# Kernel tuning notes

Measured on AMD Instinct MI355X. Metric: run time of the kernel, lower is better.

## Reference

```python
import jax, jax.numpy as jnp
import numpy as np

HEADS = 8
DIM_HEAD = 64
DIM = 512
CTX_DIM = 512
INNER = HEADS * DIM_HEAD  # 512
EPS = 1e-5


def layernorm(x, g):
    # repo-style LayerNorm: learnable gain g only, no bias, biased variance
    mean = jnp.mean(x, axis=-1, keepdims=True)
    var = jnp.var(x, axis=-1, keepdims=True)
    return (x - mean) * jax.lax.rsqrt(var + EPS) * g


def setup_inputs() -> dict:
    key = jax.random.key(0)
    ks = jax.random.split(key, 8)
    b, n, m = 2, 4096, 4096
    x = jax.random.normal(ks[0], (b, n, DIM), dtype=jnp.float32)
    context = jax.random.normal(ks[1], (b, m, CTX_DIM), dtype=jnp.float32)
    mask = jax.random.bernoulli(ks[2], 0.9, (b, m))  # bool [b, m]
    # parameters
    g_x = jnp.ones((DIM,), dtype=jnp.float32)
    null_kv = jax.random.normal(ks[3], (2, DIM_HEAD), dtype=jnp.float32)
    Wq = jax.random.normal(ks[4], (DIM, INNER), dtype=jnp.float32) * (DIM ** -0.5)
    Wkv = jax.random.normal(ks[5], (CTX_DIM, 2 * INNER), dtype=jnp.float32) * (CTX_DIM ** -0.5)
    Wo = jax.random.normal(ks[6], (INNER, DIM), dtype=jnp.float32) * (INNER ** -0.5)
    g_out = jnp.ones((DIM,), dtype=jnp.float32)
    return {"x": x, "context": context, "mask": mask, "g_x": g_x,
            "null_kv": null_kv, "Wq": Wq, "Wkv": Wkv, "Wo": Wo, "g_out": g_out}


def reference(x, context, mask, g_x, null_kv, Wq, Wkv, Wo, g_out):
    b, n, _ = x.shape
    m = context.shape[1]
    scale = DIM_HEAD ** (-0.5)  # cosine_sim=False

    xn = layernorm(x, g_x)
    ctx = context  # norm_context=False -> Identity

    q = (xn @ Wq).reshape(b, n, HEADS, DIM_HEAD)          # b n h d
    kv = (ctx @ Wkv).reshape(b, m, 2, HEADS, DIM_HEAD)     # b m 2 h d
    k, v = kv[:, :, 0], kv[:, :, 1]                        # b m h d

    # prepend the null kv token (shared across b, h)
    nk = jnp.broadcast_to(null_kv[0], (b, 1, HEADS, DIM_HEAD))
    nv = jnp.broadcast_to(null_kv[1], (b, 1, HEADS, DIM_HEAD))
    k = jnp.concatenate([nk, k], axis=1)                   # b (m+1) h d
    v = jnp.concatenate([nv, v], axis=1)

    s = jnp.sqrt(jnp.float32(scale))
    q = q * s
    k = k * s

    sim = jnp.einsum('bihd,bjhd->bhij', q, k)              # b h n (m+1)
    max_neg = -jnp.finfo(sim.dtype).max
    full_mask = jnp.pad(mask, ((0, 0), (1, 0)), constant_values=True)  # null token visible
    sim = jnp.where(full_mask[:, None, None, :], sim, max_neg)

    attn = jax.nn.softmax(sim.astype(jnp.float32), axis=-1).astype(sim.dtype)
    out = jnp.einsum('bhij,bjhd->bihd', attn, v).reshape(b, n, INNER)
    out = out @ Wo
    return layernorm(out, g_out)
```

## Files before the change

### kernel.cpp

```cpp
#include <hip/hip_runtime.h>
#include <cfloat>

typedef unsigned short u16;
typedef unsigned int u32;
typedef __bf16 v8bf16 __attribute__((ext_vector_type(8)));
typedef float v4f32 __attribute__((ext_vector_type(4)));
typedef float v16f32 __attribute__((ext_vector_type(16)));

#define MPAD 4224
#define QKS 0.42466090f
#define GRPS 1024

__device__ __forceinline__ u16 f2bf(float f) {
  union { float f; u32 u; } v; v.f = f;
  u32 u = v.u;
  u32 r = (u + 0x7FFFu + ((u >> 16) & 1u)) >> 16;
  return (u16)r;
}

__device__ __forceinline__ u32 pkbf(float lo, float hi) {
  union { float f; u32 u; } a, c;
  a.f = lo; c.f = hi;
  return __builtin_amdgcn_perm(c.u, a.u, 0x07060302);
}

__device__ __forceinline__ float asf(u32 u) {
  union { u32 u; float f; } v; v.u = u; return v.f;
}

__device__ __forceinline__ void exppack2(v16f32& sA, v16f32& sB, float& lst,
                                         v8bf16 pf[4]) {
  float rsum = 0.f;
#pragma unroll
  for (int i = 0; i < 16; i++) { float p = __builtin_amdgcn_exp2f(sA[i]); sA[i] = p; rsum += p; }
#pragma unroll
  for (int i = 0; i < 16; i++) { float p = __builtin_amdgcn_exp2f(sB[i]); sB[i] = p; rsum += p; }
  float a2 = rsum, b2 = rsum;
  asm("v_permlane32_swap_b32 %0, %1" : "+v"(a2), "+v"(b2));
  lst += a2 + b2;
#pragma unroll
  for (int kc = 0; kc < 2; kc++) {
    v16f32& s = kc ? sB : sA;
#pragma unroll
    for (int s16 = 0; s16 < 2; s16++) {
      u32 w0 = pkbf(s[s16 * 8 + 0], s[s16 * 8 + 1]);
      u32 w1 = pkbf(s[s16 * 8 + 2], s[s16 * 8 + 3]);
      u32 w2 = pkbf(s[s16 * 8 + 4], s[s16 * 8 + 5]);
      u32 w3 = pkbf(s[s16 * 8 + 6], s[s16 * 8 + 7]);
      asm("v_permlane32_swap_b32 %0, %1" : "+v"(w0), "+v"(w2));
      asm("v_permlane32_swap_b32 %0, %1" : "+v"(w1), "+v"(w3));
      union { u32 u[4]; v8bf16 v; } pu;
      pu.u[0] = w0; pu.u[1] = w1; pu.u[2] = w2; pu.u[3] = w3;
      pf[kc * 2 + s16] = pu.v;
    }
  }
}

__global__ __launch_bounds__(256) void transpose_cast3(const float* __restrict__ Wq,
    const float* __restrict__ Wkv, const float* __restrict__ Wo,
    u16* __restrict__ WqT, u16* __restrict__ WkvT, u16* __restrict__ WoT) {
  __shared__ float tile[32][33];
  int bb = blockIdx.x;
  const float* in; u16* out; int N; float scale; int base;
  if (bb < 256)      { in = Wq;  out = WqT;  N = 512;  scale = QKS; base = bb; }
  else if (bb < 768) { in = Wkv; out = WkvT; N = 1024; scale = 1.f; base = bb - 256; }
  else               { in = Wo;  out = WoT;  N = 512;  scale = 1.f; base = bb - 768; }
  const int K = 512;
  int ntiles = N >> 5;
  int bx = base % ntiles, by = base / ntiles;
  int n0 = bx * 32, k0 = by * 32;
  int c = threadIdx.x & 31, r8 = threadIdx.x >> 5;
#pragma unroll
  for (int i = 0; i < 4; i++) {
    int r = r8 + i * 8;
    tile[r][c] = in[(size_t)(k0 + r) * N + n0 + c];
  }
  __syncthreads();
#pragma unroll
  for (int i = 0; i < 4; i++) {
    int r = r8 + i * 8;
    out[(size_t)(n0 + r) * K + k0 + c] = f2bf(tile[c][r] * scale);
  }
}

__global__ __launch_bounds__(256) void ln_to_bf16(const float* __restrict__ in,
    const float* __restrict__ g, u16* __restrict__ out) {
  int lane = threadIdx.x & 63, w = threadIdx.x >> 6;
  int row = blockIdx.x * 4 + w;
  const float* p = in + (size_t)row * 512 + lane * 8;
  float4 f0 = *(const float4*)p;
  float4 f1 = *(const float4*)(p + 4);
  float v[8] = {f0.x, f0.y, f0.z, f0.w, f1.x, f1.y, f1.z, f1.w};
  float sum = 0.f, sq = 0.f;
#pragma unroll
  for (int i = 0; i < 8; i++) { sum += v[i]; sq += v[i] * v[i]; }
#pragma unroll
  for (int m = 1; m < 64; m <<= 1) { sum += __shfl_xor(sum, m); sq += __shfl_xor(sq, m); }
  float mean = sum * (1.f / 512.f);
  float var = sq * (1.f / 512.f) - mean * mean;
  float rstd = rsqrtf(var + 1e-5f);
  const float* gp = g + lane * 8;
  u16 o[8];
#pragma unroll
  for (int i = 0; i < 8; i++) o[i] = f2bf((v[i] - mean) * rstd * gp[i]);
  *(uint4*)&out[(size_t)row * 512 + lane * 8] = *(uint4*)o;
}

__global__ __launch_bounds__(256) void ln_to_f32(const float* __restrict__ in,
    const float* __restrict__ g, float* __restrict__ out) {
  int lane = threadIdx.x & 63, w = threadIdx.x >> 6;
  int row = blockIdx.x * 4 + w;
  const float* p = in + (size_t)row * 512 + lane * 8;
  float4 f0 = *(const float4*)p;
  float4 f1 = *(const float4*)(p + 4);
  float v[8] = {f0.x, f0.y, f0.z, f0.w, f1.x, f1.y, f1.z, f1.w};
  float sum = 0.f, sq = 0.f;
#pragma unroll
  for (int i = 0; i < 8; i++) { sum += v[i]; sq += v[i] * v[i]; }
#pragma unroll
  for (int m = 1; m < 64; m <<= 1) { sum += __shfl_xor(sum, m); sq += __shfl_xor(sq, m); }
  float mean = sum * (1.f / 512.f);
  float var = sq * (1.f / 512.f) - mean * mean;
  float rstd = rsqrtf(var + 1e-5f);
  const float* gp = g + lane * 8;
  float o[8];
#pragma unroll
  for (int i = 0; i < 8; i++) o[i] = (v[i] - mean) * rstd * gp[i];
  float* q = out + (size_t)row * 512 + lane * 8;
  *(float4*)q = make_float4(o[0], o[1], o[2], o[3]);
  *(float4*)(q + 4) = make_float4(o[4], o[5], o[6], o[7]);
}

__global__ __launch_bounds__(256) void cast_f32_bf16(const float4* __restrict__ in,
    u16* __restrict__ out, int n4) {
  int i = blockIdx.x * 256 + threadIdx.x;
  if (i >= n4) return;
  float4 f = in[i];
  u16 o[4] = {f2bf(f.x), f2bf(f.y), f2bf(f.z), f2bf(f.w)};
  *(uint2*)&out[i * 4] = *(uint2*)o;
}

__global__ void detect_mask_dtype(const unsigned char* __restrict__ m, int* __restrict__ flag) {
  int i = blockIdx.x * 256 + threadIdx.x;
  if (i < 8192 && (i & 3) && m[i]) atomicOr(flag, 1);
}

__global__ void build_maskpad(const void* __restrict__ mask, const int* __restrict__ flag,
    float* __restrict__ mp) {
  int i = blockIdx.x * 256 + threadIdx.x;
  if (i >= 2 * MPAD) return;
  int b = i / MPAD, p = i - b * MPAD;
  float v;
  if (p == 0) v = 0.f;
  else if (p <= 4096) {
    int j = b * 4096 + (p - 1);
    int on = (*flag) ? (((const unsigned char*)mask)[j] != 0)
                     : (((const int*)mask)[j] != 0);
    v = on ? 0.f : -1e38f;
  } else v = -1e38f;
  mp[i] = v;
}

__global__ __launch_bounds__(256) void fill_extras(const float* __restrict__ nullkv,
    u16* __restrict__ KVt) {
  int bh = blockIdx.x, tid = threadIdx.x;
  size_t tb64 = ((size_t)bh * 66 + 64) * 8192;
  uint4 z = make_uint4(0, 0, 0, 0);
  for (int i = tid; i < 2048; i += 256)
    *(uint4*)&KVt[tb64 + (size_t)i * 8] = z;
  size_t tb0 = (size_t)bh * 66 * 8192;
  if (tid < 64) {
    int d = tid;
    KVt[tb0 + (size_t)(d >> 3) * 512 + (d & 7)] = f2bf(nullkv[d] * QKS);
    KVt[tb0 + 4096 + (size_t)d * 8] = f2bf(nullkv[64 + d]);
  }
}

__global__ __launch_bounds__(256) void gemm_bf16(const u16* __restrict__ A,
    const u16* __restrict__ Bt, u16* __restrict__ outb, float* __restrict__ outf,
    u16* __restrict__ KVt, int Ncols, int mode) {
  __shared__ __attribute__((aligned(16))) u16 As[128 * 32];
  __shared__ __attribute__((aligned(16))) u16 Bs[128 * 32];
  int tiles_n = Ncols >> 7;
  int n0 = (blockIdx.x % tiles_n) * 128;
  int m0 = (blockIdx.x / tiles_n) * 128;
  int tid = threadIdx.x;
  int lane = tid & 63, w = tid >> 6, quad = lane >> 4, l15 = lane & 15;
  int wr = w >> 1, wc = w & 1;
  int srow = tid >> 2, scol = (tid & 3) * 8;
  v4f32 acc[4][4];
#pragma unroll
  for (int i = 0; i < 4; i++)
#pragma unroll
    for (int j = 0; j < 4; j++) acc[i][j] = (v4f32){0.f, 0.f, 0.f, 0.f};

  for (int k0 = 0; k0 < 512; k0 += 32) {
    __syncthreads();
    __builtin_amdgcn_global_load_lds((const u32*)&A[(size_t)(m0 + srow) * 512 + k0 + scol],
                                     (u32*)&As[tid * 8], 16, 0, 0);
    __builtin_amdgcn_global_load_lds((const u32*)&A[(size_t)(m0 + 64 + srow) * 512 + k0 + scol],
                                     (u32*)&As[64 * 32 + tid * 8], 16, 0, 0);
    __builtin_amdgcn_global_load_lds((const u32*)&Bt[(size_t)(n0 + srow) * 512 + k0 + scol],
                                     (u32*)&Bs[tid * 8], 16, 0, 0);
    __builtin_amdgcn_global_load_lds((const u32*)&Bt[(size_t)(n0 + 64 + srow) * 512 + k0 + scol],
                                     (u32*)&Bs[64 * 32 + tid * 8], 16, 0, 0);
    __syncthreads();
    v8bf16 af[4], bf[4];
#pragma unroll
    for (int i = 0; i < 4; i++)
      af[i] = *(const v8bf16*)&As[(wr * 64 + i * 16 + l15) * 32 + quad * 8];
#pragma unroll
    for (int j = 0; j < 4; j++)
      bf[j] = *(const v8bf16*)&Bs[(wc * 64 + j * 16 + l15) * 32 + quad * 8];
#pragma unroll
    for (int i = 0; i < 4; i++)
#pragma unroll
      for (int j = 0; j < 4; j++)
        acc[i][j] = __builtin_amdgcn_mfma_f32_16x16x32_bf16(af[i], bf[j], acc[i][j], 0, 0, 0);
  }
#pragma unroll
  for (int i = 0; i < 4; i++) {
    int rbase = m0 + wr * 64 + i * 16 + quad * 4;
#pragma unroll
    for (int j = 0; j < 4; j++) {
      int col = n0 + wc * 64 + j * 16 + l15;
#pragma unroll
      for (int r = 0; r < 4; r++) {
        float v = acc[i][j][r];
        int row = rbase + r;
        if (mode == 0) {
          outb[(size_t)row * 512 + col] = f2bf(v);
        } else if (mode == 2) {
          outf[(size_t)row * 512 + col] = v;
        } else {
          int b2 = row >> 12, mr = row & 4095;
          int kk = mr + 1, kt = kk >> 6, kl = kk & 63;
          int kvsel = col >> 9, hh = (col >> 6) & 7, d = col & 63;
          size_t tb = ((size_t)(b2 * 8 + hh) * 66 + kt) * 8192;
          if (kvsel == 0) {
            int chunk = (((d >> 4) * 2 + ((d >> 3) & 1)) * 2 + (kl >> 5)) * 32 + (kl & 31);
            KVt[tb + (size_t)chunk * 8 + (d & 7)] = f2bf(v * QKS);
          } else {
            int chunk = (((kl >> 4) * 2 + ((kl >> 3) & 1)) * 2 + (d >> 5)) * 32 + (d & 31);
            KVt[tb + 4096 + (size_t)chunk * 8 + (kl & 7)] = f2bf(v);
          }
        }
      }
    }
  }
}

__global__ __launch_bounds__(256, 2) void attn_kernel(const u16* __restrict__ q,
    const u16* __restrict__ KVt, const float* __restrict__ maskbias,
    u32* __restrict__ Opart, float* __restrict__ lbuf) {
  int bid = blockIdx.x;
  int qt = bid & 15, bhs = bid >> 4;
  int s_p = bhs & 1, bh = bhs >> 1;
  int b = bh >> 3, hh = bh & 7;
  int tid = threadIdx.x, lane = tid & 63, w = tid >> 6;
  int m31 = lane & 31, h = (lane >> 5) & 1;
  int grp = (bh * 16 + qt) * 4 + w;
  int q0 = qt * 256 + w * 64;

  v8bf16 qf[2][4];
#pragma unroll
  for (int qg = 0; qg < 2; qg++) {
    const u16* qp = q + (size_t)(b * 4096 + q0 + qg * 32 + m31) * 512 + hh * 64 + h * 8;
#pragma unroll
    for (int ks = 0; ks < 4; ks++) qf[qg][ks] = *(const v8bf16*)&qp[ks * 16];
  }

  v16f32 acc[2][2];
#pragma unroll
  for (int qg = 0; qg < 2; qg++)
#pragma unroll
    for (int db = 0; db < 2; db++)
#pragma unroll
      for (int i = 0; i < 16; i++) acc[qg][db][i] = 0.f;
  float l_st[2] = {0.f, 0.f};

  const u16* kvb = KVt + (size_t)bh * 66 * 8192 + (size_t)(h * 64 + m31) * 8;
  const float* mg = maskbias + b * MPAD;
  int kt0 = s_p * 33;

  v8bf16 kf[4][2];
  v16f32 bs0, bs1;
  {
    const u16* tb0 = kvb + (size_t)kt0 * 8192;
#pragma unroll
    for (int ks = 0; ks < 4; ks++)
#pragma unroll
      for (int kc = 0; kc < 2; kc++)
        kf[ks][kc] = *(const v8bf16*)&tb0[ks * 1024 + kc * 256];
#pragma unroll
    for (int gg = 0; gg < 4; gg++) {
      float4 b0 = *(const float4*)&mg[kt0 * 64 + gg * 8 + h * 4];
      float4 b1 = *(const float4*)&mg[kt0 * 64 + 32 + gg * 8 + h * 4];
      bs0[gg * 4 + 0] = b0.x; bs0[gg * 4 + 1] = b0.y; bs0[gg * 4 + 2] = b0.z; bs0[gg * 4 + 3] = b0.w;
      bs1[gg * 4 + 0] = b1.x; bs1[gg * 4 + 1] = b1.y; bs1[gg * 4 + 2] = b1.z; bs1[gg * 4 + 3] = b1.w;
    }
  }

  for (int kt = kt0; kt < kt0 + 33; ++kt) {
    const u16* tb = kvb + (size_t)kt * 8192;
    int ktn = (kt + 1 < kt0 + 33) ? kt + 1 : kt0;
    const u16* tbn = kvb + (size_t)ktn * 8192;

    v8bf16 pf[2][4];

    v16f32 s0 = bs0, s1 = bs1;
#pragma unroll
    for (int ks = 0; ks < 4; ks++) {
      s0 = __builtin_amdgcn_mfma_f32_32x32x16_bf16(kf[ks][0], qf[0][ks], s0, 0, 0, 0);
      s1 = __builtin_amdgcn_mfma_f32_32x32x16_bf16(kf[ks][1], qf[0][ks], s1, 0, 0, 0);
    }

    v8bf16 vf[4][2];
#pragma unroll
    for (int jb = 0; jb < 4; jb++)
#pragma unroll
      for (int db = 0; db < 2; db++)
        vf[jb][db] = *(const v8bf16*)&tb[4096 + jb * 1024 + db * 256];

    exppack2(s0, s1, l_st[0], pf[0]);

#pragma unroll
    for (int ks = 0; ks < 4; ks++) {
      bs0 = __builtin_amdgcn_mfma_f32_32x32x16_bf16(kf[ks][0], qf[1][ks], bs0, 0, 0, 0);
      bs1 = __builtin_amdgcn_mfma_f32_32x32x16_bf16(kf[ks][1], qf[1][ks], bs1, 0, 0, 0);
    }

    v8bf16 kfn[4][2];
#pragma unroll
    for (int ks = 0; ks < 4; ks++)
#pragma unroll
      for (int kc = 0; kc < 2; kc++)
        kfn[ks][kc] = *(const v8bf16*)&tbn[ks * 1024 + kc * 256];
    v16f32 nb0, nb1;
#pragma unroll
    for (int gg = 0; gg < 4; gg++) {
      float4 b0 = *(const float4*)&mg[ktn * 64 + gg * 8 + h * 4];
      float4 b1 = *(const float4*)&mg[ktn * 64 + 32 + gg * 8 + h * 4];
      nb0[gg * 4 + 0] = b0.x; nb0[gg * 4 + 1] = b0.y; nb0[gg * 4 + 2] = b0.z; nb0[gg * 4 + 3] = b0.w;
      nb1[gg * 4 + 0] = b1.x; nb1[gg * 4 + 1] = b1.y; nb1[gg * 4 + 2] = b1.z; nb1[gg * 4 + 3] = b1.w;
    }

    exppack2(bs0, bs1, l_st[1], pf[1]);

#pragma unroll
    for (int qg = 0; qg < 2; qg++)
#pragma unroll
      for (int jb = 0; jb < 4; jb++)
#pragma unroll
        for (int db = 0; db < 2; db++)
          acc[qg][db] = __builtin_amdgcn_mfma_f32_32x32x16_bf16(vf[jb][db], pf[qg][jb], acc[qg][db], 0, 0, 0);

#pragma unroll
    for (int ks = 0; ks < 4; ks++)
#pragma unroll
      for (int kc = 0; kc < 2; kc++)
        kf[ks][kc] = kfn[ks][kc];
    bs0 = nb0; bs1 = nb1;
  }

  size_t ob = (size_t)(s_p * GRPS + grp) * 2048;
#pragma unroll
  for (int qg = 0; qg < 2; qg++)
#pragma unroll
    for (int db = 0; db < 2; db++)
#pragma unroll
      for (int rp = 0; rp < 8; rp++)
        Opart[ob + qg * 1024 + (size_t)(db * 8 + rp) * 64 + lane] =
            pkbf(acc[qg][db][2 * rp], acc[qg][db][2 * rp + 1]);
  if (h == 0) {
    lbuf[(size_t)(s_p * GRPS + grp) * 64 + m31] = l_st[0];
    lbuf[(size_t)(s_p * GRPS + grp) * 64 + 32 + m31] = l_st[1];
  }
}

__global__ __launch_bounds__(256) void attn_combine(const u32* __restrict__ Opart,
    const float* __restrict__ lbuf, u16* __restrict__ attnO) {
  __shared__ __attribute__((aligned(16))) u16 tl[4][2176];
  int tid = threadIdx.x, lane = tid & 63, w4 = tid >> 6;
  int m31 = lane & 31, h = (lane >> 5) & 1;
  int gq = blockIdx.x * 4 + w4;
  int qg = gq & 1, grp = gq >> 1;
  int w = grp & 3, qt = (grp >> 2) & 15, bh = grp >> 6;
  int b = bh >> 3, hh = bh & 7;

  float l0 = lbuf[(size_t)grp * 64 + qg * 32 + m31];
  float l1 = lbuf[(size_t)(GRPS + grp) * 64 + qg * 32 + m31];
  float inv = 1.f / (l0 + l1);

#pragma unroll
  for (int db = 0; db < 2; db++)
#pragma unroll
    for (int rp = 0; rp < 8; rp++) {
      u32 a = Opart[(size_t)grp * 2048 + qg * 1024 + (db * 8 + rp) * 64 + lane];
      u32 c = Opart[(size_t)(GRPS + grp) * 2048 + qg * 1024 + (db * 8 + rp) * 64 + lane];
      float fe = (asf(a << 16) + asf(c << 16)) * inv;
      float fo = (asf(a & 0xFFFF0000u) + asf(c & 0xFFFF0000u)) * inv;
      int reg = 2 * rp;
      int d0 = (reg & 3) + 8 * (reg >> 2) + 4 * h + 32 * db;
      *(u32*)&tl[w4][m31 * 68 + d0] = pkbf(fe, fo);
    }
  __builtin_amdgcn_s_waitcnt(0);
  int q0 = qt * 256 + w * 64 + qg * 32;
#pragma unroll
  for (int t2 = 0; t2 < 4; t2++) {
    int row = t2 * 8 + (lane >> 3), ch = lane & 7;
    uint4 val = *(uint4*)&tl[w4][row * 68 + ch * 8];
    *(uint4*)&attnO[(size_t)(b * 4096 + q0 + row) * 512 + hh * 64 + ch * 8] = val;
  }
}

extern "C" void kernel_launch(void* const* d_in, const int* in_sizes, int n_in,
                              void* d_out, int out_size, void* d_ws, size_t ws_size,
                              hipStream_t stream) {
  const float* x       = (const float*)d_in[0];
  const float* context = (const float*)d_in[1];
  const void*  mask    = d_in[2];
  const float* g_x     = (const float*)d_in[3];
  const float* null_kv = (const float*)d_in[4];
  const float* Wq      = (const float*)d_in[5];
  const float* Wkv     = (const float*)d_in[6];
  const float* Wo      = (const float*)d_in[7];
  const float* g_out   = (const float*)d_in[8];

  char* w = (char*)d_ws;
  size_t off = 0;
  auto alloc = [&](size_t bytes) { size_t o = off; off = (off + bytes + 255) & ~(size_t)255; return o; };

  u16* WqT    = (u16*)(w + alloc((size_t)512 * 512 * 2));
  u16* WkvT   = (u16*)(w + alloc((size_t)1024 * 512 * 2));
  u16* WoT    = (u16*)(w + alloc((size_t)512 * 512 * 2));
  float* mp   = (float*)(w + alloc((size_t)2 * MPAD * 4));
  int* flag   = (int*)(w + alloc(256));
  u16* KVt    = (u16*)(w + alloc((size_t)16 * 66 * 8192 * 2));
  u16* qb     = (u16*)(w + alloc((size_t)8192 * 512 * 2));
  u16* aO     = (u16*)(w + alloc((size_t)8192 * 512 * 2));
  size_t xn_off = alloc((size_t)8192 * 512 * 2);
  size_t cb_off = alloc((size_t)8192 * 512 * 2);
  float* lbb  = (float*)(w + alloc((size_t)2 * GRPS * 64 * 4));
  u16* xn   = (u16*)(w + xn_off);
  u16* cb   = (u16*)(w + cb_off);
  u32* Opart = (u32*)(w + xn_off);
  float* OP  = (float*)(w + xn_off);

  hipMemsetAsync(flag, 0, 4, stream);
  detect_mask_dtype<<<32, 256, 0, stream>>>((const unsigned char*)mask, flag);
  build_maskpad<<<(2 * MPAD + 255) / 256, 256, 0, stream>>>(mask, flag, mp);

  transpose_cast3<<<1024, 256, 0, stream>>>(Wq, Wkv, Wo, WqT, WkvT, WoT);

  ln_to_bf16<<<2048, 256, 0, stream>>>(x, g_x, xn);
  cast_f32_bf16<<<4096, 256, 0, stream>>>((const float4*)context, cb, 8192 * 512 / 4);
  fill_extras<<<16, 256, 0, stream>>>(null_kv, KVt);

  gemm_bf16<<<(8192 / 128) * (512 / 128), 256, 0, stream>>>(xn, WqT, qb, nullptr, nullptr, 512, 0);
  gemm_bf16<<<(8192 / 128) * (1024 / 128), 256, 0, stream>>>(cb, WkvT, nullptr, nullptr, KVt, 1024, 1);

  attn_kernel<<<512, 256, 0, stream>>>(qb, KVt, mp, Opart, lbb);
  attn_combine<<<512, 256, 0, stream>>>(Opart, lbb, aO);

  gemm_bf16<<<(8192 / 128) * (512 / 128), 256, 0, stream>>>(aO, WoT, nullptr, OP, nullptr, 512, 2);
  ln_to_f32<<<2048, 256, 0, stream>>>(OP, g_out, (float*)d_out);
}
```

Measured before the change: 278.9 us.

## Merge prep kernels, fuse Q/KV GEMMs, drop attention prefetch, remap attention blocks

Seven small preprocessing launches plus a memset are merged into one multi-role kernel, and each block now detects the mask dtype locally instead of using a global atomic flag. The Q and KV projection GEMMs become a single launch. The attention kernel drops its software prefetch of the next K tile and mask bias, loading them inside the loop instead, and remaps block indices so neighbouring blocks spread across batch/head. The aim is to cut launch overhead and improve scheduling, at the risk of exposing load latency in the attention loop.

```diff
diff --git a/kernel.cpp b/kernel.cpp
--- a/kernel.cpp
+++ b/kernel.cpp
@@ -56,54 +56,106 @@
   }
 }
 
-__global__ __launch_bounds__(256) void transpose_cast3(const float* __restrict__ Wq,
-    const float* __restrict__ Wkv, const float* __restrict__ Wo,
-    u16* __restrict__ WqT, u16* __restrict__ WkvT, u16* __restrict__ WoT) {
-  __shared__ float tile[32][33];
+__global__ __launch_bounds__(256) void prep_all(
+    const void* __restrict__ mask, float* __restrict__ mp,
+    const float* __restrict__ Wq, const float* __restrict__ Wkv,
+    const float* __restrict__ Wo, u16* __restrict__ WqT,
+    u16* __restrict__ WkvT, u16* __restrict__ WoT,
+    const float* __restrict__ x, const float* __restrict__ g,
+    u16* __restrict__ xn, const float4* __restrict__ ctx, u16* __restrict__ cb,
+    const float* __restrict__ nullkv, u16* __restrict__ KVt) {
   int bb = blockIdx.x;
-  const float* in; u16* out; int N; float scale; int base;
-  if (bb < 256)      { in = Wq;  out = WqT;  N = 512;  scale = QKS; base = bb; }
-  else if (bb < 768) { in = Wkv; out = WkvT; N = 1024; scale = 1.f; base = bb - 256; }
-  else               { in = Wo;  out = WoT;  N = 512;  scale = 1.f; base = bb - 768; }
-  const int K = 512;
-  int ntiles = N >> 5;
-  int bx = base % ntiles, by = base / ntiles;
-  int n0 = bx * 32, k0 = by * 32;
-  int c = threadIdx.x & 31, r8 = threadIdx.x >> 5;
-#pragma unroll
-  for (int i = 0; i < 4; i++) {
-    int r = r8 + i * 8;
-    tile[r][c] = in[(size_t)(k0 + r) * N + n0 + c];
-  }
-  __syncthreads();
-#pragma unroll
-  for (int i = 0; i < 4; i++) {
-    int r = r8 + i * 8;
-    out[(size_t)(n0 + r) * K + k0 + c] = f2bf(tile[c][r] * scale);
-  }
-}
-
-__global__ __launch_bounds__(256) void ln_to_bf16(const float* __restrict__ in,
-    const float* __restrict__ g, u16* __restrict__ out) {
-  int lane = threadIdx.x & 63, w = threadIdx.x >> 6;
-  int row = blockIdx.x * 4 + w;
-  const float* p = in + (size_t)row * 512 + lane * 8;
-  float4 f0 = *(const float4*)p;
-  float4 f1 = *(const float4*)(p + 4);
-  float v[8] = {f0.x, f0.y, f0.z, f0.w, f1.x, f1.y, f1.z, f1.w};
-  float sum = 0.f, sq = 0.f;
-#pragma unroll
-  for (int i = 0; i < 8; i++) { sum += v[i]; sq += v[i] * v[i]; }
-#pragma unroll
-  for (int m = 1; m < 64; m <<= 1) { sum += __shfl_xor(sum, m); sq += __shfl_xor(sq, m); }
-  float mean = sum * (1.f / 512.f);
-  float var = sq * (1.f / 512.f) - mean * mean;
-  float rstd = rsqrtf(var + 1e-5f);
-  const float* gp = g + lane * 8;
-  u16 o[8];
-#pragma unroll
-  for (int i = 0; i < 8; i++) o[i] = f2bf((v[i] - mean) * rstd * gp[i]);
-  *(uint4*)&out[(size_t)row * 512 + lane * 8] = *(uint4*)o;
+  int tid = threadIdx.x;
+  if (bb < 33) {
+    __shared__ int sflag;
+    if (tid == 0) sflag = 0;
+    __syncthreads();
+    const unsigned char* mb = (const unsigned char*)mask;
+    int loc = 0;
+#pragma unroll
+    for (int k = 0; k < 32; k++) {
+      int i = tid * 32 + k;
+      if ((i & 3) && mb[i]) loc = 1;
+    }
+    if (loc) sflag = 1;
+    __syncthreads();
+    int isbyte = sflag;
+    int i = bb * 256 + tid;
+    if (i >= 2 * MPAD) return;
+    int b = i / MPAD, p = i - b * MPAD;
+    float v;
+    if (p == 0) v = 0.f;
+    else if (p <= 4096) {
+      int j = b * 4096 + (p - 1);
+      int on = isbyte ? (((const unsigned char*)mask)[j] != 0)
+                      : (((const int*)mask)[j] != 0);
+      v = on ? 0.f : -1e38f;
+    } else v = -1e38f;
+    mp[i] = v;
+  } else if (bb < 1057) {
+    __shared__ float tile[32][33];
+    int t = bb - 33;
+    const float* in; u16* out; int N; float scale; int base;
+    if (t < 256)      { in = Wq;  out = WqT;  N = 512;  scale = QKS; base = t; }
+    else if (t < 768) { in = Wkv; out = WkvT; N = 1024; scale = 1.f; base = t - 256; }
+    else              { in = Wo;  out = WoT;  N = 512;  scale = 1.f; base = t - 768; }
+    const int K = 512;
+    int ntiles = N >> 5;
+    int bx = base % ntiles, by = base / ntiles;
+    int n0 = bx * 32, k0 = by * 32;
+    int c = tid & 31, r8 = tid >> 5;
+#pragma unroll
+    for (int i = 0; i < 4; i++) {
+      int r = r8 + i * 8;
+      tile[r][c] = in[(size_t)(k0 + r) * N + n0 + c];
+    }
+    __syncthreads();
+#pragma unroll
+    for (int i = 0; i < 4; i++) {
+      int r = r8 + i * 8;
+      out[(size_t)(n0 + r) * K + k0 + c] = f2bf(tile[c][r] * scale);
+    }
+  } else if (bb < 7201) {
+    int local = bb - 1057;
+    if (local < 2048) {
+      int lane = tid & 63, w = tid >> 6;
+      int row = local * 4 + w;
+      const float* p = x + (size_t)row * 512 + lane * 8;
+      float4 f0 = *(const float4*)p;
+      float4 f1 = *(const float4*)(p + 4);
+      float v[8] = {f0.x, f0.y, f0.z, f0.w, f1.x, f1.y, f1.z, f1.w};
+      float sum = 0.f, sq = 0.f;
+#pragma unroll
+      for (int i = 0; i < 8; i++) { sum += v[i]; sq += v[i] * v[i]; }
+#pragma unroll
+      for (int m = 1; m < 64; m <<= 1) { sum += __shfl_xor(sum, m); sq += __shfl_xor(sq, m); }
+      float mean = sum * (1.f / 512.f);
+      float var = sq * (1.f / 512.f) - mean * mean;
+      float rstd = rsqrtf(var + 1e-5f);
+      const float* gp = g + lane * 8;
+      u16 o[8];
+#pragma unroll
+      for (int i = 0; i < 8; i++) o[i] = f2bf((v[i] - mean) * rstd * gp[i]);
+      *(uint4*)&xn[(size_t)row * 512 + lane * 8] = *(uint4*)o;
+    } else {
+      int i = (local - 2048) * 256 + tid;
+      float4 f = ctx[i];
+      u16 o[4] = {f2bf(f.x), f2bf(f.y), f2bf(f.z), f2bf(f.w)};
+      *(uint2*)&cb[(size_t)i * 4] = *(uint2*)o;
+    }
+  } else {
+    int bh = bb - 7201;
+    size_t tb64 = ((size_t)bh * 66 + 64) * 8192;
+    uint4 z = make_uint4(0, 0, 0, 0);
+    for (int i = tid; i < 2048; i += 256)
+      *(uint4*)&KVt[tb64 + (size_t)i * 8] = z;
+    size_t tb0 = (size_t)bh * 66 * 8192;
+    if (tid < 64) {
+      int d = tid;
+      KVt[tb0 + (size_t)(d >> 3) * 512 + (d & 7)] = f2bf(nullkv[d] * QKS);
+      KVt[tb0 + 4096 + (size_t)d * 8] = f2bf(nullkv[64 + d]);
+    }
+  }
 }
 
 __global__ __launch_bounds__(256) void ln_to_f32(const float* __restrict__ in,
@@ -131,59 +183,13 @@
   *(float4*)(q + 4) = make_float4(o[4], o[5], o[6], o[7]);
 }
 
-__global__ __launch_bounds__(256) void cast_f32_bf16(const float4* __restrict__ in,
-    u16* __restrict__ out, int n4) {
-  int i = blockIdx.x * 256 + threadIdx.x;
-  if (i >= n4) return;
-  float4 f = in[i];
-  u16 o[4] = {f2bf(f.x), f2bf(f.y), f2bf(f.z), f2bf(f.w)};
-  *(uint2*)&out[i * 4] = *(uint2*)o;
-}
-
-__global__ void detect_mask_dtype(const unsigned char* __restrict__ m, int* __restrict__ flag) {
-  int i = blockIdx.x * 256 + threadIdx.x;
-  if (i < 8192 && (i & 3) && m[i]) atomicOr(flag, 1);
-}
-
-__global__ void build_maskpad(const void* __restrict__ mask, const int* __restrict__ flag,
-    float* __restrict__ mp) {
-  int i = blockIdx.x * 256 + threadIdx.x;
-  if (i >= 2 * MPAD) return;
-  int b = i / MPAD, p = i - b * MPAD;
-  float v;
-  if (p == 0) v = 0.f;
-  else if (p <= 4096) {
-    int j = b * 4096 + (p - 1);
-    int on = (*flag) ? (((const unsigned char*)mask)[j] != 0)
-                     : (((const int*)mask)[j] != 0);
-    v = on ? 0.f : -1e38f;
-  } else v = -1e38f;
-  mp[i] = v;
-}
-
-__global__ __launch_bounds__(256) void fill_extras(const float* __restrict__ nullkv,
-    u16* __restrict__ KVt) {
-  int bh = blockIdx.x, tid = threadIdx.x;
-  size_t tb64 = ((size_t)bh * 66 + 64) * 8192;
-  uint4 z = make_uint4(0, 0, 0, 0);
-  for (int i = tid; i < 2048; i += 256)
-    *(uint4*)&KVt[tb64 + (size_t)i * 8] = z;
-  size_t tb0 = (size_t)bh * 66 * 8192;
-  if (tid < 64) {
-    int d = tid;
-    KVt[tb0 + (size_t)(d >> 3) * 512 + (d & 7)] = f2bf(nullkv[d] * QKS);
-    KVt[tb0 + 4096 + (size_t)d * 8] = f2bf(nullkv[64 + d]);
-  }
-}
-
-__global__ __launch_bounds__(256) void gemm_bf16(const u16* __restrict__ A,
+__device__ __forceinline__ void gemm_core(const u16* __restrict__ A,
     const u16* __restrict__ Bt, u16* __restrict__ outb, float* __restrict__ outf,
-    u16* __restrict__ KVt, int Ncols, int mode) {
-  __shared__ __attribute__((aligned(16))) u16 As[128 * 32];
-  __shared__ __attribute__((aligned(16))) u16 Bs[128 * 32];
+    u16* __restrict__ KVt, int Ncols, int mode, int bidx,
+    u16* As , u16* Bs ) {
   int tiles_n = Ncols >> 7;
-  int n0 = (blockIdx.x % tiles_n) * 128;
-  int m0 = (blockIdx.x / tiles_n) * 128;
+  int n0 = (bidx % tiles_n) * 128;
+  int m0 = (bidx / tiles_n) * 128;
   int tid = threadIdx.x;
   int lane = tid & 63, w = tid >> 6, quad = lane >> 4, l15 = lane & 15;
   int wr = w >> 1, wc = w & 1;
@@ -250,10 +256,29 @@
   }
 }
 
+__global__ __launch_bounds__(256) void gemm_qkv(const u16* __restrict__ xn,
+    const u16* __restrict__ WqT, u16* __restrict__ qb,
+    const u16* __restrict__ cb, const u16* __restrict__ WkvT,
+    u16* __restrict__ KVt) {
+  __shared__ __attribute__((aligned(16))) u16 As[128 * 32];
+  __shared__ __attribute__((aligned(16))) u16 Bs[128 * 32];
+  int bb = blockIdx.x;
+  if (bb < 256) gemm_core(xn, WqT, qb, nullptr, nullptr, 512, 0, bb, As, Bs);
+  else          gemm_core(cb, WkvT, nullptr, nullptr, KVt, 1024, 1, bb - 256, As, Bs);
+}
+
+__global__ __launch_bounds__(256) void gemm_o(const u16* __restrict__ aO,
+    const u16* __restrict__ WoT, float* __restrict__ OP) {
+  __shared__ __attribute__((aligned(16))) u16 As[128 * 32];
+  __shared__ __attribute__((aligned(16))) u16 Bs[128 * 32];
+  gemm_core(aO, WoT, nullptr, OP, nullptr, 512, 2, blockIdx.x, As, Bs);
+}
+
 __global__ __launch_bounds__(256, 2) void attn_kernel(const u16* __restrict__ q,
     const u16* __restrict__ KVt, const float* __restrict__ maskbias,
     u32* __restrict__ Opart, float* __restrict__ lbuf) {
-  int bid = blockIdx.x;
+  int obid = blockIdx.x;
+  int bid = (obid & 7) * 64 + (obid >> 3);
   int qt = bid & 15, bhs = bid >> 4;
   int s_p = bhs & 1, bh = bhs >> 1;
   int b = bh >> 3, hh = bh & 7;
@@ -283,37 +308,42 @@
   const float* mg = maskbias + b * MPAD;
   int kt0 = s_p * 33;
 
-  v8bf16 kf[4][2];
-  v16f32 bs0, bs1;
-  {
-    const u16* tb0 = kvb + (size_t)kt0 * 8192;
-#pragma unroll
-    for (int ks = 0; ks < 4; ks++)
-#pragma unroll
-      for (int kc = 0; kc < 2; kc++)
-        kf[ks][kc] = *(const v8bf16*)&tb0[ks * 1024 + kc * 256];
-#pragma unroll
-    for (int gg = 0; gg < 4; gg++) {
-      float4 b0 = *(const float4*)&mg[kt0 * 64 + gg * 8 + h * 4];
-      float4 b1 = *(const float4*)&mg[kt0 * 64 + 32 + gg * 8 + h * 4];
-      bs0[gg * 4 + 0] = b0.x; bs0[gg * 4 + 1] = b0.y; bs0[gg * 4 + 2] = b0.z; bs0[gg * 4 + 3] = b0.w;
-      bs1[gg * 4 + 0] = b1.x; bs1[gg * 4 + 1] = b1.y; bs1[gg * 4 + 2] = b1.z; bs1[gg * 4 + 3] = b1.w;
-    }
-  }
-
   for (int kt = kt0; kt < kt0 + 33; ++kt) {
     const u16* tb = kvb + (size_t)kt * 8192;
-    int ktn = (kt + 1 < kt0 + 33) ? kt + 1 : kt0;
-    const u16* tbn = kvb + (size_t)ktn * 8192;
+    v8bf16 kf[4][2];
+#pragma unroll
+    for (int ks = 0; ks < 4; ks++)
+#pragma unroll
+      for (int kc = 0; kc < 2; kc++)
+        kf[ks][kc] = *(const v8bf16*)&tb[ks * 1024 + kc * 256];
+    v16f32 bias_s[2];
+#pragma unroll
+    for (int kc = 0; kc < 2; kc++)
+#pragma unroll
+      for (int gg = 0; gg < 4; gg++) {
+        float4 bv = *(const float4*)&mg[kt * 64 + kc * 32 + gg * 8 + h * 4];
+        bias_s[kc][gg * 4 + 0] = bv.x;
+        bias_s[kc][gg * 4 + 1] = bv.y;
+        bias_s[kc][gg * 4 + 2] = bv.z;
+        bias_s[kc][gg * 4 + 3] = bv.w;
+      }
 
     v8bf16 pf[2][4];
-
-    v16f32 s0 = bs0, s1 = bs1;
+    {
+      v16f32 s0 = bias_s[0], s1 = bias_s[1];
+#pragma unroll
+      for (int ks = 0; ks < 4; ks++) {
+        s0 = __builtin_amdgcn_mfma_f32_32x32x16_bf16(kf[ks][0], qf[0][ks], s0, 0, 0, 0);
+        s1 = __builtin_amdgcn_mfma_f32_32x32x16_bf16(kf[ks][1], qf[0][ks], s1, 0, 0, 0);
+      }
+      exppack2(s0, s1, l_st[0], pf[0]);
+    }
 #pragma unroll
     for (int ks = 0; ks < 4; ks++) {
-      s0 = __builtin_amdgcn_mfma_f32_32x32x16_bf16(kf[ks][0], qf[0][ks], s0, 0, 0, 0);
-      s1 = __builtin_amdgcn_mfma_f32_32x32x16_bf16(kf[ks][1], qf[0][ks], s1, 0, 0, 0);
-    }
+      bias_s[0] = __builtin_amdgcn_mfma_f32_32x32x16_bf16(kf[ks][0], qf[1][ks], bias_s[0], 0, 0, 0);
+      bias_s[1] = __builtin_amdgcn_mfma_f32_32x32x16_bf16(kf[ks][1], qf[1][ks], bias_s[1], 0, 0, 0);
+    }
+    exppack2(bias_s[0], bias_s[1], l_st[1], pf[1]);
 
     v8bf16 vf[4][2];
 #pragma unroll
@@ -322,31 +352,6 @@
       for (int db = 0; db < 2; db++)
         vf[jb][db] = *(const v8bf16*)&tb[4096 + jb * 1024 + db * 256];
 
-    exppack2(s0, s1, l_st[0], pf[0]);
-
-#pragma unroll
-    for (int ks = 0; ks < 4; ks++) {
-      bs0 = __builtin_amdgcn_mfma_f32_32x32x16_bf16(kf[ks][0], qf[1][ks], bs0, 0, 0, 0);
-      bs1 = __builtin_amdgcn_mfma_f32_32x32x16_bf16(kf[ks][1], qf[1][ks], bs1, 0, 0, 0);
-    }
-
-    v8bf16 kfn[4][2];
-#pragma unroll
-    for (int ks = 0; ks < 4; ks++)
-#pragma unroll
-      for (int kc = 0; kc < 2; kc++)
-        kfn[ks][kc] = *(const v8bf16*)&tbn[ks * 1024 + kc * 256];
-    v16f32 nb0, nb1;
-#pragma unroll
-    for (int gg = 0; gg < 4; gg++) {
-      float4 b0 = *(const float4*)&mg[ktn * 64 + gg * 8 + h * 4];
-      float4 b1 = *(const float4*)&mg[ktn * 64 + 32 + gg * 8 + h * 4];
-      nb0[gg * 4 + 0] = b0.x; nb0[gg * 4 + 1] = b0.y; nb0[gg * 4 + 2] = b0.z; nb0[gg * 4 + 3] = b0.w;
-      nb1[gg * 4 + 0] = b1.x; nb1[gg * 4 + 1] = b1.y; nb1[gg * 4 + 2] = b1.z; nb1[gg * 4 + 3] = b1.w;
-    }
-
-    exppack2(bs0, bs1, l_st[1], pf[1]);
-
 #pragma unroll
     for (int qg = 0; qg < 2; qg++)
 #pragma unroll
@@ -354,13 +359,6 @@
 #pragma unroll
         for (int db = 0; db < 2; db++)
           acc[qg][db] = __builtin_amdgcn_mfma_f32_32x32x16_bf16(vf[jb][db], pf[qg][jb], acc[qg][db], 0, 0, 0);
-
-#pragma unroll
-    for (int ks = 0; ks < 4; ks++)
-#pragma unroll
-      for (int kc = 0; kc < 2; kc++)
-        kf[ks][kc] = kfn[ks][kc];
-    bs0 = nb0; bs1 = nb1;
   }
 
   size_t ob = (size_t)(s_p * GRPS + grp) * 2048;
@@ -435,7 +433,6 @@
   u16* WkvT   = (u16*)(w + alloc((size_t)1024 * 512 * 2));
   u16* WoT    = (u16*)(w + alloc((size_t)512 * 512 * 2));
   float* mp   = (float*)(w + alloc((size_t)2 * MPAD * 4));
-  int* flag   = (int*)(w + alloc(256));
   u16* KVt    = (u16*)(w + alloc((size_t)16 * 66 * 8192 * 2));
   u16* qb     = (u16*)(w + alloc((size_t)8192 * 512 * 2));
   u16* aO     = (u16*)(w + alloc((size_t)8192 * 512 * 2));
@@ -447,22 +444,15 @@
   u32* Opart = (u32*)(w + xn_off);
   float* OP  = (float*)(w + xn_off);
 
-  hipMemsetAsync(flag, 0, 4, stream);
-  detect_mask_dtype<<<32, 256, 0, stream>>>((const unsigned char*)mask, flag);
-  build_maskpad<<<(2 * MPAD + 255) / 256, 256, 0, stream>>>(mask, flag, mp);
-
-  transpose_cast3<<<1024, 256, 0, stream>>>(Wq, Wkv, Wo, WqT, WkvT, WoT);
-
-  ln_to_bf16<<<2048, 256, 0, stream>>>(x, g_x, xn);
-  cast_f32_bf16<<<4096, 256, 0, stream>>>((const float4*)context, cb, 8192 * 512 / 4);
-  fill_extras<<<16, 256, 0, stream>>>(null_kv, KVt);
-
-  gemm_bf16<<<(8192 / 128) * (512 / 128), 256, 0, stream>>>(xn, WqT, qb, nullptr, nullptr, 512, 0);
-  gemm_bf16<<<(8192 / 128) * (1024 / 128), 256, 0, stream>>>(cb, WkvT, nullptr, nullptr, KVt, 1024, 1);
+  prep_all<<<7217, 256, 0, stream>>>(mask, mp, Wq, Wkv, Wo, WqT, WkvT, WoT,
+                                     x, g_x, xn, (const float4*)context, cb,
+                                     null_kv, KVt);
+
+  gemm_qkv<<<768, 256, 0, stream>>>(xn, WqT, qb, cb, WkvT, KVt);
 
   attn_kernel<<<512, 256, 0, stream>>>(qb, KVt, mp, Opart, lbb);
   attn_combine<<<512, 256, 0, stream>>>(Opart, lbb, aO);
 
-  gemm_bf16<<<(8192 / 128) * (512 / 128), 256, 0, stream>>>(aO, WoT, nullptr, OP, nullptr, 512, 2);
+  gemm_o<<<(8192 / 128) * (512 / 128), 256, 0, stream>>>(aO, WoT, OP);
   ln_to_f32<<<2048, 256, 0, stream>>>(OP, g_out, (float*)d_out);
 }
```

Result: faster. 236.7 us (-15.1%).
